# Kernel tuning notes

Hardware: AMD Instinct MI355X
Metric: run time of the kernel (lower is better)

The kernel has to match this reference:

```python
import jax, jax.numpy as jnp
import numpy as np

D = 512
H = 8
DH = D // H
EPS = 1e-5


def _layernorm(x, g, b):
    mu = jnp.mean(x, axis=-1, keepdims=True)
    var = jnp.mean((x - mu) ** 2, axis=-1, keepdims=True)
    return (x - mu) * jax.lax.rsqrt(var + EPS) * g + b


def setup_inputs() -> dict:
    key = jax.random.key(0)
    ks = jax.random.split(key, 10)
    B, S = 4, 2048
    s = 1.0 / np.sqrt(D)
    return {
        "x": jax.random.normal(ks[0], (B, S, D), dtype=jnp.float32),
        "Wq": jax.random.normal(ks[1], (D, D), dtype=jnp.float32) * s,
        "Wk": jax.random.normal(ks[2], (D, D), dtype=jnp.float32) * s,
        "Wv": jax.random.normal(ks[3], (D, D), dtype=jnp.float32) * s,
        "Wo": jax.random.normal(ks[4], (D, D), dtype=jnp.float32) * s,
        "W1": jax.random.normal(ks[5], (4 * D, D), dtype=jnp.float32) * s,
        "b1": jnp.zeros((4 * D,), dtype=jnp.float32),
        "W2": jax.random.normal(ks[6], (D, 4 * D), dtype=jnp.float32) * (1.0 / np.sqrt(4 * D)),
        "b2": jnp.zeros((D,), dtype=jnp.float32),
        "g1": jnp.ones((D,), dtype=jnp.float32),
        "bb1": jnp.zeros((D,), dtype=jnp.float32),
        "g2": jnp.ones((D,), dtype=jnp.float32),
        "bb2": jnp.zeros((D,), dtype=jnp.float32),
    }


def reference(x, Wq, Wk, Wv, Wo, W1, b1, W2, b2, g1, bb1, g2, bb2):
    B, S, _ = x.shape
    # projections (torch Linear: y = x @ W.T), split heads: chunk(-1) == reshape to [B,S,H,DH]
    q = (x @ Wq.T).reshape(B, S, H, DH).transpose(0, 2, 1, 3)  # [B,H,S,DH]
    k = (x @ Wk.T).reshape(B, S, H, DH).transpose(0, 2, 1, 3)
    v = (x @ Wv.T).reshape(B, S, H, DH).transpose(0, 2, 1, 3)
    scores = jnp.einsum("bhsd,bhtd->bhst", q, k) / np.sqrt(DH)  # [B,H,S,S]
    attn = jax.nn.softmax(scores, axis=-1)
    ctx = jnp.einsum("bhst,bhtd->bhsd", attn, v)  # [B,H,S,DH]
    ctx = ctx.transpose(0, 2, 1, 3).reshape(B, S, D)
    h = _layernorm(x + ctx @ Wo.T, g1, bb1)
    mlp = jax.nn.relu(h @ W1.T + b1) @ W2.T + b2
    return _layernorm(h + mlp, g2, bb2)
```

## Files before the change

kernel.cpp:

```cpp
#include <hip/hip_runtime.h>
#include <hip/hip_bf16.h>
#include <cstdint>
#include <cstddef>

typedef short bf16x8 __attribute__((ext_vector_type(8)));
typedef float floatx4 __attribute__((ext_vector_type(4)));
typedef unsigned int uintx4 __attribute__((ext_vector_type(4)));
typedef unsigned short u16;

constexpr int B = 4, S = 2048, D = 512, H = 8, DH = 64;
constexpr int M_ROWS = B * S;
constexpr int D4 = 4 * D;
constexpr float QSCALE = 0.18033688011112042f;

__device__ __forceinline__ u16 f2b(float f) {
  unsigned u = __builtin_bit_cast(unsigned, f);
  u += 0x7fff + ((u >> 16) & 1);
  return (u16)(u >> 16);
}

__device__ __forceinline__ bf16x8 ldfrag(const u16* p) {
  return *reinterpret_cast<const bf16x8*>(p);
}

__device__ __forceinline__ floatx4 mfma16(bf16x8 a, bf16x8 b, floatx4 c) {
  return __builtin_amdgcn_mfma_f32_16x16x32_bf16(a, b, c, 0, 0, 0);
}

__device__ __forceinline__ ushort4 f2b4(float4 v) {
  ushort4 r;
  r.x = f2b(v.x); r.y = f2b(v.y); r.z = f2b(v.z); r.w = f2b(v.w);
  return r;
}

__device__ __forceinline__ void gld16(const u16* g, u16* l) {
  __builtin_amdgcn_global_load_lds(
      (const __attribute__((address_space(1))) void*)g,
      (__attribute__((address_space(3))) void*)l, 16, 0, 0);
}

__global__ void cast_all_kernel(const float4* __restrict__ x,
                                const float4* __restrict__ w1, const float4* __restrict__ w2,
                                const float4* __restrict__ wq, const float4* __restrict__ wk,
                                const float4* __restrict__ wv, const float4* __restrict__ wo,
                                ushort4* __restrict__ xb,
                                ushort4* __restrict__ w1b, ushort4* __restrict__ w2b,
                                ushort4* __restrict__ wqb, ushort4* __restrict__ wkb,
                                ushort4* __restrict__ wvb, ushort4* __restrict__ wob) {
  int i = blockIdx.x * blockDim.x + threadIdx.x;
  constexpr int NX = (M_ROWS * D) / 4;
  constexpr int N1 = (D4 * D) / 4;
  constexpr int NS = (D * D) / 4;
  if (i < NX) { xb[i] = f2b4(x[i]); return; }
  i -= NX;
  if (i < N1) { w1b[i] = f2b4(w1[i]); return; }
  i -= N1;
  if (i < N1) { w2b[i] = f2b4(w2[i]); return; }
  i -= N1;
  const int sel = i >> 16, off = i & (NS - 1);
  const float4* src = sel == 0 ? wq : sel == 1 ? wk : sel == 2 ? wv : wo;
  ushort4* dst = sel == 0 ? wqb : sel == 1 ? wkb : sel == 2 ? wvb : wob;
  dst[off] = f2b4(src[off]);
}

template <int EPI>
__global__ __launch_bounds__(256) void gemm_bt(
    const u16* __restrict__ A, const u16* __restrict__ W,
    const float* __restrict__ bias, void* __restrict__ out0, void* __restrict__ out1,
    int M, int N, int K, int klen) {
  __shared__ __align__(16) u16 As[2][128 * 32];
  __shared__ __align__(16) u16 Bs[2][128 * 32];
  const int wave = threadIdx.x >> 6, lane = threadIdx.x & 63;
  const int quad = lane >> 4, l16 = lane & 15;
  const int rowB = blockIdx.y * 128, colB = blockIdx.x * 128;
  const int rowW = (wave >> 1) * 64, colW = (wave & 1) * 64;
  const int koff = blockIdx.z * klen;
  void* out = blockIdx.z ? out1 : out0;

  floatx4 acc[4][4];
#pragma unroll
  for (int i = 0; i < 4; i++)
#pragma unroll
    for (int j = 0; j < 4; j++) acc[i][j] = (floatx4){0.f,0.f,0.f,0.f};

  const u16* gA = A + (size_t)(rowB + wave * 32 + (lane >> 2)) * K + koff + (lane & 3) * 8;
  const u16* gB = W + (size_t)(colB + wave * 32 + (lane >> 2)) * K + koff + (lane & 3) * 8;
  const int lds_off = wave * 1024;

#pragma unroll
  for (int rr = 0; rr < 2; rr++) {
    gld16(gA + (size_t)rr * 16 * K, &As[0][lds_off + rr * 512]);
    gld16(gB + (size_t)rr * 16 * K, &Bs[0][lds_off + rr * 512]);
  }

  int buf = 0;
  for (int kc = 0; kc < klen; kc += 32, buf ^= 1) {
    __syncthreads();

    if (kc + 32 < klen) {
#pragma unroll
      for (int rr = 0; rr < 2; rr++) {
        gld16(gA + (size_t)rr * 16 * K + kc + 32, &As[buf ^ 1][lds_off + rr * 512]);
        gld16(gB + (size_t)rr * 16 * K + kc + 32, &Bs[buf ^ 1][lds_off + rr * 512]);
      }
    }

    bf16x8 a[4], b[4];
#pragma unroll
    for (int i = 0; i < 4; i++)
      a[i] = ldfrag(&As[buf][(rowW + i * 16 + l16) * 32 + quad * 8]);
#pragma unroll
    for (int j = 0; j < 4; j++)
      b[j] = ldfrag(&Bs[buf][(colW + j * 16 + l16) * 32 + quad * 8]);
#pragma unroll
    for (int i = 0; i < 4; i++)
#pragma unroll
      for (int j = 0; j < 4; j++) acc[i][j] = mfma16(a[i], b[j], acc[i][j]);
  }

#pragma unroll
  for (int i = 0; i < 4; i++) {
#pragma unroll
    for (int j = 0; j < 4; j++) {
      const int gn = colB + colW + j * 16 + l16;
      const float bv = (EPI == 1) ? bias[gn] : 0.f;
#pragma unroll
      for (int r = 0; r < 4; r++) {
        const int gm = rowB + rowW + i * 16 + quad * 4 + r;
        float v = acc[i][j][r] + bv;
        if (EPI == 0) {
          ((float*)out)[(size_t)gm * N + gn] = v;
        } else {
          v = v > 0.f ? v : 0.f;
          ((u16*)out)[(size_t)gm * N + gn] = f2b(v);
        }
      }
    }
  }
}

__global__ __launch_bounds__(256) void qkv_gemm(
    const u16* __restrict__ xb,
    const u16* __restrict__ wq, const u16* __restrict__ wk, const u16* __restrict__ wv,
    u16* __restrict__ q, u16* __restrict__ k, u16* __restrict__ vT) {
  __shared__ __align__(16) u16 As[2][128 * 32];
  __shared__ __align__(16) u16 Bs[2][128 * 32];
  const int which = blockIdx.z;
  const u16* __restrict__ W = which == 0 ? wq : (which == 1 ? wk : wv);
  const int wave = threadIdx.x >> 6, lane = threadIdx.x & 63;
  const int quad = lane >> 4, l16 = lane & 15;
  const int rowB = blockIdx.y * 128, colB = blockIdx.x * 128;
  const int rowW = (wave >> 1) * 64, colW = (wave & 1) * 64;

  floatx4 acc[4][4];
#pragma unroll
  for (int i = 0; i < 4; i++)
#pragma unroll
    for (int j = 0; j < 4; j++) acc[i][j] = (floatx4){0.f,0.f,0.f,0.f};

  const u16* gA = xb + (size_t)(rowB + wave * 32 + (lane >> 2)) * D + (lane & 3) * 8;
  const u16* gB = W + (size_t)(colB + wave * 32 + (lane >> 2)) * D + (lane & 3) * 8;
  const int lds_off = wave * 1024;

#pragma unroll
  for (int rr = 0; rr < 2; rr++) {
    gld16(gA + (size_t)rr * 16 * D, &As[0][lds_off + rr * 512]);
    gld16(gB + (size_t)rr * 16 * D, &Bs[0][lds_off + rr * 512]);
  }

  int buf = 0;
  for (int kc = 0; kc < D; kc += 32, buf ^= 1) {
    __syncthreads();

    if (kc + 32 < D) {
#pragma unroll
      for (int rr = 0; rr < 2; rr++) {
        gld16(gA + (size_t)rr * 16 * D + kc + 32, &As[buf ^ 1][lds_off + rr * 512]);
        gld16(gB + (size_t)rr * 16 * D + kc + 32, &Bs[buf ^ 1][lds_off + rr * 512]);
      }
    }

    bf16x8 a[4], b[4];
#pragma unroll
    for (int i = 0; i < 4; i++)
      a[i] = ldfrag(&As[buf][(rowW + i * 16 + l16) * 32 + quad * 8]);
#pragma unroll
    for (int j = 0; j < 4; j++)
      b[j] = ldfrag(&Bs[buf][(colW + j * 16 + l16) * 32 + quad * 8]);
#pragma unroll
    for (int i = 0; i < 4; i++)
#pragma unroll
      for (int j = 0; j < 4; j++) acc[i][j] = mfma16(a[i], b[j], acc[i][j]);
  }

  const float oscale = (which == 0) ? QSCALE : 1.0f;
  u16* dst01 = which == 0 ? q : k;
#pragma unroll
  for (int i = 0; i < 4; i++) {
#pragma unroll
    for (int j = 0; j < 4; j++) {
      const int gn = colB + colW + j * 16 + l16;
      const int h = gn >> 6, dh = gn & 63;
#pragma unroll
      for (int r = 0; r < 4; r++) {
        const int gm = rowB + rowW + i * 16 + quad * 4 + r;
        const int bb = gm >> 11, s = gm & 2047;
        const u16 val = f2b(acc[i][j][r] * oscale);
        if (which < 2) {
          dst01[((((size_t)bb * H + h) * S) + s) * DH + dh] = val;
        } else {
          const int sl = s & 63;
          const int sw = (s & ~63) | (sl & 35) | ((sl & 12) << 1) | ((sl & 16) >> 2);
          vT[((((size_t)bb * H + h) * DH) + dh) * S + sw] = val;
        }
      }
    }
  }
}

__global__ __launch_bounds__(512, 1) void attn_kernel(
    const u16* __restrict__ q, const u16* __restrict__ k,
    const u16* __restrict__ vT, u16* __restrict__ ctxb) {
  __shared__ __align__(16) u16 kvbuf[3][2][2][2][64 * 32];
  __shared__ __align__(16) float ltb[2][4][64];
  const int wave = threadIdx.x >> 6, lane = threadIdx.x & 63;
  const int quad = lane >> 4, l16 = lane & 15;
  const int pair = wave >> 1, khalf = wave & 1;
  const int blk = (blockIdx.x & 7) * 32 + (blockIdx.x >> 3);
  const int w = blk * 4 + pair;
  const int bh = w >> 5, qt = w & 31;
  const int bb = bh >> 3, h = bh & 7;

  const u16* qp = q + ((size_t)bh * S + qt * 64 + l16) * DH + quad * 8;
  bf16x8 qf[4][2];
#pragma unroll
  for (int t = 0; t < 4; t++) {
    qf[t][0] = ldfrag(qp + (size_t)t * 16 * DH);
    qf[t][1] = ldfrag(qp + (size_t)t * 16 * DH + 32);
  }

  const int st = pair * 64 + lane;
  const int srow = st >> 2, sp = (st & 3) * 8;
  const u16* kS = k + (size_t)bh * S * DH + (size_t)(khalf * 1024 + srow) * DH + sp;
  const u16* vS = vT + (size_t)bh * DH * S + (size_t)srow * S + khalf * 1024 + sp;

  floatx4 o[4][4];
#pragma unroll
  for (int t = 0; t < 4; t++)
#pragma unroll
    for (int c = 0; c < 4; c++) o[t][c] = (floatx4){0.f,0.f,0.f,0.f};
  float lacc[4] = {0.f, 0.f, 0.f, 0.f};

#pragma unroll
  for (int T = 0; T < 2; T++) {
    gld16(kS + (size_t)T * 64 * DH,      &kvbuf[T][khalf][0][0][pair * 512]);
    gld16(kS + (size_t)T * 64 * DH + 32, &kvbuf[T][khalf][0][1][pair * 512]);
    gld16(vS + T * 64,                   &kvbuf[T][khalf][1][0][pair * 512]);
    gld16(vS + T * 64 + 32,              &kvbuf[T][khalf][1][1][pair * 512]);
  }

  int rb = 0, wb = 2;
  for (int it = 0; it < 16; ++it) {
    if (it < 15) asm volatile("s_waitcnt vmcnt(4)" ::: "memory");
    else         asm volatile("s_waitcnt vmcnt(0)" ::: "memory");
    __builtin_amdgcn_s_barrier();
    __builtin_amdgcn_sched_barrier(0);

    if (it + 2 < 16) {
      gld16(kS + (size_t)(it + 2) * 64 * DH,      &kvbuf[wb][khalf][0][0][pair * 512]);
      gld16(kS + (size_t)(it + 2) * 64 * DH + 32, &kvbuf[wb][khalf][0][1][pair * 512]);
      gld16(vS + (it + 2) * 64,                   &kvbuf[wb][khalf][1][0][pair * 512]);
      gld16(vS + (it + 2) * 64 + 32,              &kvbuf[wb][khalf][1][1][pair * 512]);
    }

    bf16x8 kf[8], vf[8];
    const u16* kb0 = &kvbuf[rb][khalf][0][0][0];
    const u16* kb1 = &kvbuf[rb][khalf][0][1][0];
    const u16* vb0 = &kvbuf[rb][khalf][1][0][0];
    const u16* vb1 = &kvbuf[rb][khalf][1][1][0];
#pragma unroll
    for (int i = 0; i < 4; i++) {
      kf[2 * i]     = ldfrag(&kb0[(i * 16 + l16) * 32 + quad * 8]);
      kf[2 * i + 1] = ldfrag(&kb1[(i * 16 + l16) * 32 + quad * 8]);
      vf[2 * i]     = ldfrag(&vb0[(i * 16 + l16) * 32 + quad * 8]);
      vf[2 * i + 1] = ldfrag(&vb1[(i * 16 + l16) * 32 + quad * 8]);
    }

#pragma unroll
    for (int t = 0; t < 4; t++) {
      floatx4 sc[4];
#pragma unroll
      for (int i = 0; i < 4; i++) {
        floatx4 z = (floatx4){0.f,0.f,0.f,0.f};
        z = mfma16(kf[2 * i], qf[t][0], z);
        z = mfma16(kf[2 * i + 1], qf[t][1], z);
        sc[i] = z;
      }

      unsigned wd[8];
      float a = 0.f;
#pragma unroll
      for (int i = 0; i < 4; i++) {
        const float p0 = __builtin_amdgcn_exp2f(sc[i][0]);
        const float p1 = __builtin_amdgcn_exp2f(sc[i][1]);
        const float p2 = __builtin_amdgcn_exp2f(sc[i][2]);
        const float p3 = __builtin_amdgcn_exp2f(sc[i][3]);
        a += (p0 + p1) + (p2 + p3);
        wd[2 * i] = __builtin_amdgcn_perm(
            __builtin_bit_cast(unsigned, p1) + 0x8000u,
            __builtin_bit_cast(unsigned, p0) + 0x8000u, 0x07060302u);
        wd[2 * i + 1] = __builtin_amdgcn_perm(
            __builtin_bit_cast(unsigned, p3) + 0x8000u,
            __builtin_bit_cast(unsigned, p2) + 0x8000u, 0x07060302u);
      }
      lacc[t] += a;
      const uintx4 lo4 = (uintx4){wd[0], wd[1], wd[2], wd[3]};
      const uintx4 hi4 = (uintx4){wd[4], wd[5], wd[6], wd[7]};
      const bf16x8 pa0 = __builtin_bit_cast(bf16x8, lo4);
      const bf16x8 pa1 = __builtin_bit_cast(bf16x8, hi4);

#pragma unroll
      for (int c = 0; c < 4; c++) {
        o[t][c] = mfma16(pa0, vf[2 * c], o[t][c]);
        o[t][c] = mfma16(pa1, vf[2 * c + 1], o[t][c]);
      }
    }

    rb = rb == 2 ? 0 : rb + 1;
    wb = wb == 2 ? 0 : wb + 1;
  }

  float lt[4];
#pragma unroll
  for (int t = 0; t < 4; t++) {
    float l = lacc[t];
    l += __shfl_xor(l, 16);
    l += __shfl_xor(l, 32);
    lt[t] = l;
  }

  __syncthreads();
  float* ob = reinterpret_cast<float*>(&kvbuf[0][0][0][0][0]) + pair * 4096;
  if (quad == 0) {
#pragma unroll
    for (int t = 0; t < 4; t++) ltb[khalf][pair][t * 16 + l16] = lt[t];
  }
  if (khalf == 1) {
#pragma unroll
    for (int t = 0; t < 4; t++)
#pragma unroll
      for (int c = 0; c < 4; c++) {
        const int idx = 4 * t + c;
        const int slot = (idx & 8) | ((idx ^ (lane & 7)) & 7);
        *reinterpret_cast<floatx4*>(&ob[lane * 64 + slot * 4]) = o[t][c];
      }
  }
  __syncthreads();
  if (khalf == 0) {
    float inv[4][4];
#pragma unroll
    for (int t = 0; t < 4; t++)
#pragma unroll
      for (int r = 0; r < 4; r++)
        inv[t][r] = 1.0f / (ltb[0][pair][t * 16 + quad * 4 + r] +
                            ltb[1][pair][t * 16 + quad * 4 + r]);

    const size_t crow_base = ((size_t)bb * S) * D + h * DH;
#pragma unroll
    for (int t = 0; t < 4; t++)
#pragma unroll
      for (int c = 0; c < 4; c++) {
        const int idx = 4 * t + c;
        const int slot = (idx & 8) | ((idx ^ (lane & 7)) & 7);
        const floatx4 oo = o[t][c] +
            *reinterpret_cast<const floatx4*>(&ob[lane * 64 + slot * 4]);
        const int dh = c * 16 + l16;
#pragma unroll
        for (int r = 0; r < 4; r++) {
          const int s = qt * 64 + t * 16 + quad * 4 + r;
          ctxb[crow_base + (size_t)s * D + dh] = f2b(oo[r] * inv[t][r]);
        }
      }
  }
}

template <int MODE>
__global__ __launch_bounds__(256) void ln_kernel(
    const void* __restrict__ resid, const float* __restrict__ ya,
    const float* __restrict__ yb, const float* __restrict__ pb,
    const float* __restrict__ g, const float* __restrict__ bvec,
    float* __restrict__ outF, u16* __restrict__ outB) {
  const int wave = threadIdx.x >> 6, lane = threadIdx.x & 63;
  const int row = blockIdx.x * 4 + wave;
  const float* ap = ya + (size_t)row * D + lane * 8;
  const float* bp = yb + (size_t)row * D + lane * 8;
  float v[8];
  const float4 a0 = *(const float4*)ap, a1 = *(const float4*)(ap + 4);
  const float4 b0 = *(const float4*)bp, b1 = *(const float4*)(bp + 4);
  v[0] = a0.x + b0.x; v[1] = a0.y + b0.y; v[2] = a0.z + b0.z; v[3] = a0.w + b0.w;
  v[4] = a1.x + b1.x; v[5] = a1.y + b1.y; v[6] = a1.z + b1.z; v[7] = a1.w + b1.w;
  if (MODE == 0) {
    const float* rp = (const float*)resid + (size_t)row * D + lane * 8;
    const float4 r0 = *(const float4*)rp, r1 = *(const float4*)(rp + 4);
    v[0] += r0.x; v[1] += r0.y; v[2] += r0.z; v[3] += r0.w;
    v[4] += r1.x; v[5] += r1.y; v[6] += r1.z; v[7] += r1.w;
  } else {
    const u16* rp = (const u16*)resid + (size_t)row * D + lane * 8;
    const ushort4 h0 = *(const ushort4*)rp, h1 = *(const ushort4*)(rp + 4);
    v[0] += __builtin_bit_cast(float, (unsigned)h0.x << 16);
    v[1] += __builtin_bit_cast(float, (unsigned)h0.y << 16);
    v[2] += __builtin_bit_cast(float, (unsigned)h0.z << 16);
    v[3] += __builtin_bit_cast(float, (unsigned)h0.w << 16);
    v[4] += __builtin_bit_cast(float, (unsigned)h1.x << 16);
    v[5] += __builtin_bit_cast(float, (unsigned)h1.y << 16);
    v[6] += __builtin_bit_cast(float, (unsigned)h1.z << 16);
    v[7] += __builtin_bit_cast(float, (unsigned)h1.w << 16);
    const float4 p0 = *(const float4*)(pb + lane * 8);
    const float4 p1 = *(const float4*)(pb + lane * 8 + 4);
    v[0] += p0.x; v[1] += p0.y; v[2] += p0.z; v[3] += p0.w;
    v[4] += p1.x; v[5] += p1.y; v[6] += p1.z; v[7] += p1.w;
  }
  float sum = 0.f;
#pragma unroll
  for (int i = 0; i < 8; i++) sum += v[i];
#pragma unroll
  for (int d = 1; d < 64; d <<= 1) sum += __shfl_xor(sum, d);
  const float mu = sum * (1.f / D);
  float vs = 0.f;
#pragma unroll
  for (int i = 0; i < 8; i++) { const float t = v[i] - mu; vs += t * t; }
#pragma unroll
  for (int d = 1; d < 64; d <<= 1) vs += __shfl_xor(vs, d);
  const float rstd = rsqrtf(vs * (1.f / D) + 1e-5f);
#pragma unroll
  for (int i = 0; i < 8; i++) {
    const int col = lane * 8 + i;
    const float o = (v[i] - mu) * rstd * g[col] + bvec[col];
    if (MODE == 0) outB[(size_t)row * D + col] = f2b(o);
    else           outF[(size_t)row * D + col] = o;
  }
}

constexpr size_t OFF_XB  = 0;
constexpr size_t OFF_WQB = 8u << 20;
constexpr size_t OFF_WKB = OFF_WQB + (512u << 10);
constexpr size_t OFF_WVB = OFF_WKB + (512u << 10);
constexpr size_t OFF_WOB = OFF_WVB + (512u << 10);
constexpr size_t OFF_W1B = 10u << 20;
constexpr size_t OFF_W2B = 12u << 20;
constexpr size_t OFF_Q   = 14u << 20;
constexpr size_t OFF_K   = 22u << 20;
constexpr size_t OFF_VT  = 30u << 20;
constexpr size_t OFF_CTX = 38u << 20;
constexpr size_t OFF_Y   = 46u << 20;
constexpr size_t OFF_HB  = 78u << 20;
constexpr size_t OFF_M1B = 86u << 20;

extern "C" void kernel_launch(void* const* d_in, const int* in_sizes, int n_in,
                              void* d_out, int out_size, void* d_ws, size_t ws_size,
                              hipStream_t stream) {
  const float* x  = (const float*)d_in[0];
  const float* Wq = (const float*)d_in[1];
  const float* Wk = (const float*)d_in[2];
  const float* Wv = (const float*)d_in[3];
  const float* Wo = (const float*)d_in[4];
  const float* W1 = (const float*)d_in[5];
  const float* b1 = (const float*)d_in[6];
  const float* W2 = (const float*)d_in[7];
  const float* b2 = (const float*)d_in[8];
  const float* g1 = (const float*)d_in[9];
  const float* bb1 = (const float*)d_in[10];
  const float* g2 = (const float*)d_in[11];
  const float* bb2 = (const float*)d_in[12];

  char* ws = (char*)d_ws;
  u16* xb  = (u16*)(ws + OFF_XB);
  u16* wqb = (u16*)(ws + OFF_WQB);
  u16* wkb = (u16*)(ws + OFF_WKB);
  u16* wvb = (u16*)(ws + OFF_WVB);
  u16* wob = (u16*)(ws + OFF_WOB);
  u16* w1b = (u16*)(ws + OFF_W1B);
  u16* w2b = (u16*)(ws + OFF_W2B);
  u16* qb  = (u16*)(ws + OFF_Q);
  u16* kb  = (u16*)(ws + OFF_K);
  u16* vtb = (u16*)(ws + OFF_VT);
  u16* ctxb = (u16*)(ws + OFF_CTX);
  float* y0 = (float*)(ws + OFF_Y);
  float* y1 = (float*)(ws + OFF_Q);
  u16* hb  = (u16*)(ws + OFF_HB);
  u16* m1b = (u16*)(ws + OFF_M1B);

  {
    const int n4 = (M_ROWS * D) / 4 + (D4 * D) / 4 * 2 + (D * D) / 4 * 4;
    cast_all_kernel<<<(n4 + 255) / 256, 256, 0, stream>>>(
        (const float4*)x, (const float4*)W1, (const float4*)W2, (const float4*)Wq,
        (const float4*)Wk, (const float4*)Wv, (const float4*)Wo,
        (ushort4*)xb, (ushort4*)w1b, (ushort4*)w2b, (ushort4*)wqb,
        (ushort4*)wkb, (ushort4*)wvb, (ushort4*)wob);
  }

  qkv_gemm<<<dim3(D / 128, M_ROWS / 128, 3), 256, 0, stream>>>(xb, wqb, wkb, wvb, qb, kb, vtb);

  attn_kernel<<<B * H * S / 64 / 4, 512, 0, stream>>>(qb, kb, vtb, ctxb);

  gemm_bt<0><<<dim3(D / 128, M_ROWS / 128, 2), 256, 0, stream>>>(
      ctxb, wob, nullptr, y0, y1, M_ROWS, D, D, D / 2);

  ln_kernel<0><<<M_ROWS / 4, 256, 0, stream>>>(
      x, y0, y1, nullptr, g1, bb1, nullptr, hb);

  gemm_bt<1><<<dim3(D4 / 128, M_ROWS / 128, 1), 256, 0, stream>>>(
      hb, w1b, b1, m1b, nullptr, M_ROWS, D4, D, D);

  gemm_bt<0><<<dim3(D / 128, M_ROWS / 128, 2), 256, 0, stream>>>(
      m1b, w2b, nullptr, y0, y1, M_ROWS, D, D4, D4 / 2);

  ln_kernel<1><<<M_ROWS / 4, 256, 0, stream>>>(
      hb, y0, y1, b2, g2, bb2, (float*)d_out, nullptr);
}
```

Before: 260.3 us.

## Triple-buffer GEMM LDS tiles with explicit vmcnt waits in QKV and split-K GEMMs

```diff
diff --git a/kernel.cpp b/kernel.cpp
--- a/kernel.cpp
+++ b/kernel.cpp
@@ -63,13 +63,13 @@
   dst[off] = f2b4(src[off]);
 }
 
-template <int EPI>
+template <int EPI, int PIPE>
 __global__ __launch_bounds__(256) void gemm_bt(
     const u16* __restrict__ A, const u16* __restrict__ W,
     const float* __restrict__ bias, void* __restrict__ out0, void* __restrict__ out1,
     int M, int N, int K, int klen) {
-  __shared__ __align__(16) u16 As[2][128 * 32];
-  __shared__ __align__(16) u16 Bs[2][128 * 32];
+  __shared__ __align__(16) u16 As[PIPE ? 3 : 2][128 * 32];
+  __shared__ __align__(16) u16 Bs[PIPE ? 3 : 2][128 * 32];
   const int wave = threadIdx.x >> 6, lane = threadIdx.x & 63;
   const int quad = lane >> 4, l16 = lane & 15;
   const int rowB = blockIdx.y * 128, colB = blockIdx.x * 128;
@@ -87,35 +87,76 @@
   const u16* gB = W + (size_t)(colB + wave * 32 + (lane >> 2)) * K + koff + (lane & 3) * 8;
   const int lds_off = wave * 1024;
 
-#pragma unroll
-  for (int rr = 0; rr < 2; rr++) {
-    gld16(gA + (size_t)rr * 16 * K, &As[0][lds_off + rr * 512]);
-    gld16(gB + (size_t)rr * 16 * K, &Bs[0][lds_off + rr * 512]);
-  }
-
-  int buf = 0;
-  for (int kc = 0; kc < klen; kc += 32, buf ^= 1) {
-    __syncthreads();
-
-    if (kc + 32 < klen) {
-#pragma unroll
-      for (int rr = 0; rr < 2; rr++) {
-        gld16(gA + (size_t)rr * 16 * K + kc + 32, &As[buf ^ 1][lds_off + rr * 512]);
-        gld16(gB + (size_t)rr * 16 * K + kc + 32, &Bs[buf ^ 1][lds_off + rr * 512]);
-      }
-    }
-
-    bf16x8 a[4], b[4];
-#pragma unroll
-    for (int i = 0; i < 4; i++)
-      a[i] = ldfrag(&As[buf][(rowW + i * 16 + l16) * 32 + quad * 8]);
-#pragma unroll
-    for (int j = 0; j < 4; j++)
-      b[j] = ldfrag(&Bs[buf][(colW + j * 16 + l16) * 32 + quad * 8]);
-#pragma unroll
-    for (int i = 0; i < 4; i++)
-#pragma unroll
-      for (int j = 0; j < 4; j++) acc[i][j] = mfma16(a[i], b[j], acc[i][j]);
+  if constexpr (PIPE) {
+    const int nt = klen / 32;
+#pragma unroll
+    for (int T = 0; T < 2; T++) {
+      gld16(gA + T * 32,                    &As[T][lds_off]);
+      gld16(gA + (size_t)16 * K + T * 32,   &As[T][lds_off + 512]);
+      gld16(gB + T * 32,                    &Bs[T][lds_off]);
+      gld16(gB + (size_t)16 * K + T * 32,   &Bs[T][lds_off + 512]);
+    }
+    int rb = 0, wb = 2;
+    for (int it = 0; it < nt; ++it) {
+      if (it + 1 < nt) asm volatile("s_waitcnt vmcnt(4)" ::: "memory");
+      else             asm volatile("s_waitcnt vmcnt(0)" ::: "memory");
+      __builtin_amdgcn_s_barrier();
+      __builtin_amdgcn_sched_barrier(0);
+
+      if (it + 2 < nt) {
+        const int kc2 = (it + 2) * 32;
+        gld16(gA + kc2,                    &As[wb][lds_off]);
+        gld16(gA + (size_t)16 * K + kc2,   &As[wb][lds_off + 512]);
+        gld16(gB + kc2,                    &Bs[wb][lds_off]);
+        gld16(gB + (size_t)16 * K + kc2,   &Bs[wb][lds_off + 512]);
+      }
+
+      bf16x8 a[4], b[4];
+#pragma unroll
+      for (int i = 0; i < 4; i++)
+        a[i] = ldfrag(&As[rb][(rowW + i * 16 + l16) * 32 + quad * 8]);
+#pragma unroll
+      for (int j = 0; j < 4; j++)
+        b[j] = ldfrag(&Bs[rb][(colW + j * 16 + l16) * 32 + quad * 8]);
+#pragma unroll
+      for (int i = 0; i < 4; i++)
+#pragma unroll
+        for (int j = 0; j < 4; j++) acc[i][j] = mfma16(a[i], b[j], acc[i][j]);
+
+      rb = rb == 2 ? 0 : rb + 1;
+      wb = wb == 2 ? 0 : wb + 1;
+    }
+  } else {
+#pragma unroll
+    for (int rr = 0; rr < 2; rr++) {
+      gld16(gA + (size_t)rr * 16 * K, &As[0][lds_off + rr * 512]);
+      gld16(gB + (size_t)rr * 16 * K, &Bs[0][lds_off + rr * 512]);
+    }
+
+    int buf = 0;
+    for (int kc = 0; kc < klen; kc += 32, buf ^= 1) {
+      __syncthreads();
+
+      if (kc + 32 < klen) {
+#pragma unroll
+        for (int rr = 0; rr < 2; rr++) {
+          gld16(gA + (size_t)rr * 16 * K + kc + 32, &As[buf ^ 1][lds_off + rr * 512]);
+          gld16(gB + (size_t)rr * 16 * K + kc + 32, &Bs[buf ^ 1][lds_off + rr * 512]);
+        }
+      }
+
+      bf16x8 a[4], b[4];
+#pragma unroll
+      for (int i = 0; i < 4; i++)
+        a[i] = ldfrag(&As[buf][(rowW + i * 16 + l16) * 32 + quad * 8]);
+#pragma unroll
+      for (int j = 0; j < 4; j++)
+        b[j] = ldfrag(&Bs[buf][(colW + j * 16 + l16) * 32 + quad * 8]);
+#pragma unroll
+      for (int i = 0; i < 4; i++)
+#pragma unroll
+        for (int j = 0; j < 4; j++) acc[i][j] = mfma16(a[i], b[j], acc[i][j]);
+    }
   }
 
 #pragma unroll
@@ -143,8 +184,8 @@
     const u16* __restrict__ xb,
     const u16* __restrict__ wq, const u16* __restrict__ wk, const u16* __restrict__ wv,
     u16* __restrict__ q, u16* __restrict__ k, u16* __restrict__ vT) {
-  __shared__ __align__(16) u16 As[2][128 * 32];
-  __shared__ __align__(16) u16 Bs[2][128 * 32];
+  __shared__ __align__(16) u16 As[3][128 * 32];
+  __shared__ __align__(16) u16 Bs[3][128 * 32];
   const int which = blockIdx.z;
   const u16* __restrict__ W = which == 0 ? wq : (which == 1 ? wk : wv);
   const int wave = threadIdx.x >> 6, lane = threadIdx.x & 63;
@@ -162,35 +203,43 @@
   const u16* gB = W + (size_t)(colB + wave * 32 + (lane >> 2)) * D + (lane & 3) * 8;
   const int lds_off = wave * 1024;
 
-#pragma unroll
-  for (int rr = 0; rr < 2; rr++) {
-    gld16(gA + (size_t)rr * 16 * D, &As[0][lds_off + rr * 512]);
-    gld16(gB + (size_t)rr * 16 * D, &Bs[0][lds_off + rr * 512]);
-  }
-
-  int buf = 0;
-  for (int kc = 0; kc < D; kc += 32, buf ^= 1) {
-    __syncthreads();
-
-    if (kc + 32 < D) {
-#pragma unroll
-      for (int rr = 0; rr < 2; rr++) {
-        gld16(gA + (size_t)rr * 16 * D + kc + 32, &As[buf ^ 1][lds_off + rr * 512]);
-        gld16(gB + (size_t)rr * 16 * D + kc + 32, &Bs[buf ^ 1][lds_off + rr * 512]);
-      }
+  constexpr int nt = D / 32;
+#pragma unroll
+  for (int T = 0; T < 2; T++) {
+    gld16(gA + T * 32,                    &As[T][lds_off]);
+    gld16(gA + (size_t)16 * D + T * 32,   &As[T][lds_off + 512]);
+    gld16(gB + T * 32,                    &Bs[T][lds_off]);
+    gld16(gB + (size_t)16 * D + T * 32,   &Bs[T][lds_off + 512]);
+  }
+  int rb = 0, wb = 2;
+  for (int it = 0; it < nt; ++it) {
+    if (it + 1 < nt) asm volatile("s_waitcnt vmcnt(4)" ::: "memory");
+    else             asm volatile("s_waitcnt vmcnt(0)" ::: "memory");
+    __builtin_amdgcn_s_barrier();
+    __builtin_amdgcn_sched_barrier(0);
+
+    if (it + 2 < nt) {
+      const int kc2 = (it + 2) * 32;
+      gld16(gA + kc2,                    &As[wb][lds_off]);
+      gld16(gA + (size_t)16 * D + kc2,   &As[wb][lds_off + 512]);
+      gld16(gB + kc2,                    &Bs[wb][lds_off]);
+      gld16(gB + (size_t)16 * D + kc2,   &Bs[wb][lds_off + 512]);
     }
 
     bf16x8 a[4], b[4];
 #pragma unroll
     for (int i = 0; i < 4; i++)
-      a[i] = ldfrag(&As[buf][(rowW + i * 16 + l16) * 32 + quad * 8]);
+      a[i] = ldfrag(&As[rb][(rowW + i * 16 + l16) * 32 + quad * 8]);
 #pragma unroll
     for (int j = 0; j < 4; j++)
-      b[j] = ldfrag(&Bs[buf][(colW + j * 16 + l16) * 32 + quad * 8]);
+      b[j] = ldfrag(&Bs[rb][(colW + j * 16 + l16) * 32 + quad * 8]);
 #pragma unroll
     for (int i = 0; i < 4; i++)
 #pragma unroll
       for (int j = 0; j < 4; j++) acc[i][j] = mfma16(a[i], b[j], acc[i][j]);
+
+    rb = rb == 2 ? 0 : rb + 1;
+    wb = wb == 2 ? 0 : wb + 1;
   }
 
   const float oscale = (which == 0) ? QSCALE : 1.0f;
@@ -503,16 +552,16 @@
 
   attn_kernel<<<B * H * S / 64 / 4, 512, 0, stream>>>(qb, kb, vtb, ctxb);
 
-  gemm_bt<0><<<dim3(D / 128, M_ROWS / 128, 2), 256, 0, stream>>>(
+  gemm_bt<0, 1><<<dim3(D / 128, M_ROWS / 128, 2), 256, 0, stream>>>(
       ctxb, wob, nullptr, y0, y1, M_ROWS, D, D, D / 2);
 
   ln_kernel<0><<<M_ROWS / 4, 256, 0, stream>>>(
       x, y0, y1, nullptr, g1, bb1, nullptr, hb);
 
-  gemm_bt<1><<<dim3(D4 / 128, M_ROWS / 128, 1), 256, 0, stream>>>(
+  gemm_bt<1, 0><<<dim3(D4 / 128, M_ROWS / 128, 1), 256, 0, stream>>>(
       hb, w1b, b1, m1b, nullptr, M_ROWS, D4, D, D);
 
-  gemm_bt<0><<<dim3(D / 128, M_ROWS / 128, 2), 256, 0, stream>>>(
+  gemm_bt<0, 1><<<dim3(D / 128, M_ROWS / 128, 2), 256, 0, stream>>>(
       m1b, w2b, nullptr, y0, y1, M_ROWS, D, D4, D4 / 2);
 
   ln_kernel<1><<<M_ROWS / 4, 256, 0, stream>>>(
```

New measurement: 257.4 us. No clear change (-1.1%).
